# Kernel optimization log

Hardware: AMD Instinct MI355X
Metric: run time of the kernel (lower is better)

## Reference

```python
import jax, jax.numpy as jnp
import numpy as np

G = 4          # num_groups == num_kv_groups


def _proj(W, b, xf):
    # 1x1 Conv3d == per-voxel linear: xf is [b, c, N]
    return jnp.einsum('oc,bcn->bon', W, xf) + b[None, :, None]


def setup_inputs() -> dict:
    key = jax.random.key(0)
    ks = jax.random.split(key, 5)
    c = 512
    x = jax.random.normal(ks[0], (2, c, 16, 16, 16), dtype=jnp.float32)
    s = 1.0 / np.sqrt(c)
    Wq = jax.random.normal(ks[1], (c, c), dtype=jnp.float32) * s
    Wk = jax.random.normal(ks[2], (c, c), dtype=jnp.float32) * s
    Wv = jax.random.normal(ks[3], (c, c), dtype=jnp.float32) * s
    Wo = jax.random.normal(ks[4], (c, c), dtype=jnp.float32) * s
    z = jnp.zeros((c,), dtype=jnp.float32)
    return {"x": x, "Wq": Wq, "bq": z, "Wk": Wk, "bk": z, "Wv": Wv, "bv": z, "Wo": Wo, "bo": z}


def reference(x, Wq, bq, Wk, bk, Wv, bv, Wo, bo):
    b, c, d, h, w = x.shape
    N = d * h * w
    gs = c // G                       # head (group) dim
    scale = gs ** -0.5
    xf = x.reshape(b, c, N)           # [b, c, N]
    q = _proj(Wq, bq, xf).reshape(b, G, gs, N).transpose(0, 1, 3, 2)  # [b,G,N,gs]
    k = _proj(Wk, bk, xf).reshape(b, G, gs, N).transpose(0, 1, 3, 2)
    v = _proj(Wv, bv, xf).reshape(b, G, gs, N).transpose(0, 1, 3, 2)
    sim = jnp.einsum('bgqd,bgkd->bgqk', q, k) * scale  # [b,G,N,N]
    attn = jax.nn.softmax(sim, axis=-1)
    out = jnp.einsum('bgqk,bgkd->bgqd', attn, v)       # [b,G,N,gs]
    out = out.transpose(0, 1, 3, 2).reshape(b, c, N)   # [b,c,N]
    out = _proj(Wo, bo, out).reshape(b, c, d, h, w)
    return x + out
```

## Files before the change

### kernel.cpp

```cpp
#include <hip/hip_runtime.h>
#include <hip/hip_bf16.h>
#include <stdint.h>

#define B_ 2
#define C_ 512
#define G_ 4
#define D_ 128
#define N_ 4096

typedef __bf16 bf16;
typedef __bf16 bf16x8 __attribute__((ext_vector_type(8)));
typedef float  f32x4  __attribute__((ext_vector_type(4)));
typedef float  f32x16 __attribute__((ext_vector_type(16)));

#define MFMA   __builtin_amdgcn_mfma_f32_16x16x32_bf16
#define MFMA32 __builtin_amdgcn_mfma_f32_32x32x16_bf16

#define SWZ(row, c) ((((c) ^ (((row) >> 1) & 3)) << 4))

#define OFF_Q   (0u)
#define OFF_K   (8388608u)
#define OFF_VT  (16777216u)
#define OFF_XT  (25165824u)
#define OFF_WB  (33554432u)
#define OFF_OP  (35651584u)
#define OFF_ML  (52428800u)
#define WS_NEED_SPLIT (52953088u)

__device__ inline unsigned pk2(float a, float b) {
    union { bf16 h[2]; unsigned u; } t;
    t.h[0] = (bf16)a; t.h[1] = (bf16)b;
    return t.u;
}
__device__ inline void pl32(unsigned &a, unsigned &b) {
    asm volatile("v_permlane32_swap_b32 %0, %1" : "+v"(a), "+v"(b));
}
__device__ inline void gload16(const char* src, char* lds) {
    __builtin_amdgcn_global_load_lds(
        (const __attribute__((address_space(1))) unsigned*)src,
        (__attribute__((address_space(3))) unsigned*)lds, 16, 0, 0);
}
__device__ inline float max3f(float a, float b, float c) {
    return fmaxf(fmaxf(a, b), c);
}

__global__ __launch_bounds__(256) void wcvt_kernel(const float* __restrict__ Wq,
                                                   const float* __restrict__ Wk,
                                                   const float* __restrict__ Wv,
                                                   const float* __restrict__ Wo,
                                                   bf16* __restrict__ out) {
    int m = blockIdx.y;
    const float* W = (m == 0) ? Wq : (m == 1) ? Wk : (m == 2) ? Wv : Wo;
    int i = (blockIdx.x * 256 + threadIdx.x) * 4;
    float4 v = *(const float4*)(W + i);
    union { bf16 h[4]; uint2 u; } pk;
    pk.h[0] = (bf16)v.x; pk.h[1] = (bf16)v.y; pk.h[2] = (bf16)v.z; pk.h[3] = (bf16)v.w;
    *(uint2*)(out + (size_t)m * (C_ * C_) + i) = pk.u;
}

__global__ __launch_bounds__(256) void xt_kernel(const float* __restrict__ x,
                                                 bf16* __restrict__ xT) {
    __shared__ bf16 t[64 * 80];
    int n0 = blockIdx.x * 64, c0 = blockIdx.y * 64, b = blockIdx.z;
    const float* xp = x + (size_t)b * C_ * N_;
#pragma unroll
    for (int i = 0; i < 16; ++i) {
        int idx = threadIdx.x + 256 * i;
        int cl = idx >> 6, nl = idx & 63;
        float v = xp[(size_t)(c0 + cl) * N_ + n0 + nl];
        t[nl * 80 + cl] = (bf16)v;
    }
    __syncthreads();
    bf16* xt = xT + ((size_t)b * N_ + n0) * C_ + c0;
#pragma unroll
    for (int i = 0; i < 2; ++i) {
        int id = threadIdx.x + 256 * i;
        int nl = id >> 3, c8 = (id & 7) * 8;
        *(uint4*)(xt + (size_t)nl * C_ + c8) = *(const uint4*)(t + nl * 80 + c8);
    }
}

__global__ __launch_bounds__(256) void qkv_kernel(const bf16* __restrict__ xT,
                                                  const bf16* __restrict__ WB,
                                                  const float* __restrict__ bq,
                                                  const float* __restrict__ bk,
                                                  const float* __restrict__ bv,
                                                  bf16* __restrict__ Q,
                                                  bf16* __restrict__ K,
                                                  bf16* __restrict__ Vt) {
    __shared__ char smem[32768];
    const int tid = threadIdx.x;
    const int w = tid >> 6, l = tid & 63;
    const int lr = l & 15, lg = l >> 4;
    const int wr = w >> 1, wc = w & 1;
    const int mat = blockIdx.z;
    const bf16* A = xT;
    const bf16* W = WB + (size_t)mat * (C_ * C_);
    const float* bias = (mat == 0) ? bq : (mat == 1) ? bk : bv;
    const int r0 = blockIdx.x * 128, o0 = blockIdx.y * 128;
    const float QSCALE = 0.08838834764831845f * 1.4426950408889634f;

    const char* srcA[2]; const char* srcB[2]; int dA[2], dB[2];
#pragma unroll
    for (int i = 0; i < 2; ++i) {
        int CL = tid + 256 * i, row = CL >> 2, c = CL & 3;
        srcA[i] = (const char*)(A + (size_t)(r0 + row) * C_) + SWZ(row, c);
        srcB[i] = (const char*)(W + (size_t)(o0 + row) * C_) + SWZ(row, c);
        dA[i] = CL << 4;
        dB[i] = 8192 + (CL << 4);
    }

    f32x4 z = {0.f, 0.f, 0.f, 0.f};
    f32x4 acc[4][4];
#pragma unroll
    for (int m = 0; m < 4; ++m)
#pragma unroll
        for (int n = 0; n < 4; ++n) acc[m][n] = z;

    auto STAGE = [&](int buf, int kt) {
        char* base = smem + buf * 16384;
        int kb = kt * 64;
#pragma unroll
        for (int i = 0; i < 2; ++i) {
            gload16(srcA[i] + kb, base + dA[i]);
            gload16(srcB[i] + kb, base + dB[i]);
        }
    };

    STAGE(0, 0);
    __syncthreads();
#pragma unroll 4
    for (int t = 0; t < 16; ++t) {
        int cur = t & 1;
        if (t < 15) STAGE(cur ^ 1, t + 1);
        char* Ab = smem + cur * 16384;
        char* Bb = Ab + 8192;
        bf16x8 af[4], bg_[4];
#pragma unroll
        for (int m = 0; m < 4; ++m) {
            int row = wr * 64 + m * 16 + lr;
            af[m] = *(const bf16x8*)(Ab + row * 64 + SWZ(row, lg));
        }
#pragma unroll
        for (int n = 0; n < 4; ++n) {
            int row = wc * 64 + n * 16 + lr;
            bg_[n] = *(const bf16x8*)(Bb + row * 64 + SWZ(row, lg));
        }
#pragma unroll
        for (int m = 0; m < 4; ++m)
#pragma unroll
            for (int n = 0; n < 4; ++n)
                acc[m][n] = MFMA(af[m], bg_[n], acc[m][n], 0, 0, 0);
        __syncthreads();
    }

#pragma unroll
    for (int n = 0; n < 4; ++n) {
        int o = o0 + wc * 64 + n * 16 + lr;
        float bs = bias[o];
        int g = o >> 7, d = o & 127;
#pragma unroll
        for (int m = 0; m < 4; ++m) {
            int row = r0 + wr * 64 + m * 16 + lg * 4;
            int b = row >> 12, nn = row & (N_ - 1);
            if (mat == 0) {
#pragma unroll
                for (int j = 0; j < 4; ++j)
                    Q[((size_t)(b * G_ + g) * N_ + nn + j) * D_ + d] =
                        (bf16)((acc[m][n][j] + bs) * QSCALE);
            } else if (mat == 1) {
#pragma unroll
                for (int j = 0; j < 4; ++j)
                    K[((size_t)(b * G_ + g) * N_ + nn + j) * D_ + d] =
                        (bf16)(acc[m][n][j] + bs);
            } else {
                union { bf16 h[4]; uint2 u; } pk;
#pragma unroll
                for (int j = 0; j < 4; ++j) pk.h[j] = (bf16)(acc[m][n][j] + bs);
                *(uint2*)(Vt + ((size_t)(b * G_ + g) * D_ + d) * N_ + nn) = pk.u;
            }
        }
    }
}

template<int SPLITS>
__global__ __launch_bounds__(256, 2) void attn_kernel(const bf16* __restrict__ Q,
                                                      const bf16* __restrict__ K,
                                                      const bf16* __restrict__ Vt,
                                                      bf16* __restrict__ XT,
                                                      bf16* __restrict__ Op,
                                                      float* __restrict__ ML) {
    __shared__ char smem[65536];
    const int tid = threadIdx.x;
    const int w = tid >> 6, l = tid & 63;
    const int l31 = l & 31, h = l >> 5;

    const int L = blockIdx.x;
    const int bg = L & 7;
    const int ix = L >> 3;
    const int sp = (SPLITS > 1) ? (ix >> 5) : 0;
    const int qb = (SPLITS > 1) ? (ix & 31) : ix;

    const bf16* Qh = Q + (size_t)bg * N_ * D_;
    const char* Kh = (const char*)(K + (size_t)bg * N_ * D_);
    const char* Vh = (const char*)(Vt + (size_t)bg * D_ * N_);
    const int q0 = qb * 128 + w * 32;
    const int kv0 = sp * (N_ / SPLITS);
    const int NT = N_ / SPLITS / 64;

    int offK[4], offV[4];
#pragma unroll
    for (int j = 0; j < 4; ++j) {
        int CL = (w * 4 + j) * 64 + l;
        int row = CL >> 4;
        int cp = (CL & 15) ^ (row & 15);
        offK[j] = row * 256 + cp * 16;
        int dv = 2 * row + (cp >> 3), k8 = cp & 7;
        offV[j] = dv * (N_ * 2) + k8 * 16;
    }

    bf16x8 aq[8];
#pragma unroll
    for (int kb = 0; kb < 8; ++kb)
        aq[kb] = *(const bf16x8*)(Qh + (size_t)(q0 + l31) * D_ + kb * 16 + h * 8);

    bf16 one_ = (bf16)1.0f;
    bf16x8 ones = {one_, one_, one_, one_, one_, one_, one_, one_};

    f32x16 oacc[4], lacc;
#pragma unroll
    for (int dt = 0; dt < 4; ++dt)
#pragma unroll
        for (int r = 0; r < 16; ++r) oacc[dt][r] = 0.f;
#pragma unroll
    for (int r = 0; r < 16; ++r) lacc[r] = 0.f;
    float mrun = -1e30f;
    const float THR = 5.0f;

    auto STAGE = [&](int buf, int kv) {
        const char* pk = Kh + (size_t)kv * 256;
        const char* pv = Vh + (size_t)kv * 2;
        char* kb = smem + buf * 32768 + w * 4096;
        char* vb = smem + buf * 32768 + 16384 + w * 4096;
#pragma unroll
        for (int j = 0; j < 4; ++j) gload16(pk + offK[j], kb + j * 1024);
#pragma unroll
        for (int j = 0; j < 4; ++j) gload16(pv + offV[j], vb + j * 1024);
    };

    STAGE(0, kv0);

    for (int t = 0; t < NT; ++t) {
        int cur = t & 1;
        __builtin_amdgcn_s_barrier();
        if (t + 1 < NT) {
            STAGE(cur ^ 1, kv0 + (t + 1) * 64);
            asm volatile("s_waitcnt vmcnt(8)" ::: "memory");
        } else {
            asm volatile("s_waitcnt vmcnt(0)" ::: "memory");
        }
        __builtin_amdgcn_sched_barrier(0);
        __builtin_amdgcn_s_barrier();
        char* Kb = smem + cur * 32768;
        char* Vb = smem + cur * 32768 + 16384;

        f32x16 s0, s1;
#pragma unroll
        for (int r = 0; r < 16; ++r) { s0[r] = 0.f; s1[r] = 0.f; }
        __builtin_amdgcn_s_setprio(1);
#pragma unroll
        for (int kb = 0; kb < 8; ++kb) {
            int ch = (((kb << 1) | h) ^ (l31 & 15)) << 4;
            bf16x8 kf0 = *(const bf16x8*)(Kb + (size_t)l31 * 256 + ch);
            s0 = MFMA32(kf0, aq[kb], s0, 0, 0, 0);
            bf16x8 kf1 = *(const bf16x8*)(Kb + (size_t)(32 + l31) * 256 + ch);
            s1 = MFMA32(kf1, aq[kb], s1, 0, 0, 0);
        }
        __builtin_amdgcn_s_setprio(0);

        float x0 = max3f(s0[0],  s0[1],  s0[2]);
        float x1 = max3f(s0[3],  s0[4],  s0[5]);
        float x2 = max3f(s0[6],  s0[7],  s0[8]);
        float x3 = max3f(s0[9],  s0[10], s0[11]);
        float x4 = max3f(s0[12], s0[13], s0[14]);
        float x5 = max3f(s0[15], s1[0],  s1[1]);
        float x6 = max3f(s1[2],  s1[3],  s1[4]);
        float x7 = max3f(s1[5],  s1[6],  s1[7]);
        float x8 = max3f(s1[8],  s1[9],  s1[10]);
        float x9 = max3f(s1[11], s1[12], s1[13]);
        float xa = fmaxf(s1[14], s1[15]);
        float y0 = max3f(x0, x1, x2);
        float y1 = max3f(x3, x4, x5);
        float y2 = max3f(x6, x7, x8);
        float y3 = fmaxf(x9, xa);
        float mt = fmaxf(max3f(y0, y1, y2), y3);
        mt = fmaxf(mt, __shfl_xor(mt, 32));

        if (__any(mt > mrun + THR)) {
            float mn = fmaxf(mrun, mt);
            float corr = __builtin_amdgcn_exp2f(mrun - mn);
            mrun = mn;
#pragma unroll
            for (int r = 0; r < 16; ++r) {
                int qr = (r & 3) + 8 * (r >> 2) + 4 * h;
                float cr = __shfl(corr, qr);
                lacc[r] *= cr;
#pragma unroll
                for (int dt = 0; dt < 4; ++dt) oacc[dt][r] *= cr;
            }
        }

#pragma unroll
        for (int r = 0; r < 16; ++r) {
            s0[r] = __builtin_amdgcn_exp2f(s0[r] - mrun);
            s1[r] = __builtin_amdgcn_exp2f(s1[r] - mrun);
        }

        bf16x8 pa0, pa1, pa2, pa3;
        {
            unsigned x0_ = pk2(s0[0], s0[1]),  y0_ = pk2(s0[4], s0[5]);  pl32(x0_, y0_);
            unsigned x1_ = pk2(s0[2], s0[3]),  y1_ = pk2(s0[6], s0[7]);  pl32(x1_, y1_);
            pa0 = __builtin_bit_cast(bf16x8, (uint4){x0_, x1_, y0_, y1_});
            unsigned x2_ = pk2(s0[8], s0[9]),  y2_ = pk2(s0[12], s0[13]); pl32(x2_, y2_);
            unsigned x3_ = pk2(s0[10], s0[11]), y3_ = pk2(s0[14], s0[15]); pl32(x3_, y3_);
            pa1 = __builtin_bit_cast(bf16x8, (uint4){x2_, x3_, y2_, y3_});
            unsigned x4_ = pk2(s1[0], s1[1]),  y4_ = pk2(s1[4], s1[5]);  pl32(x4_, y4_);
            unsigned x5_ = pk2(s1[2], s1[3]),  y5_ = pk2(s1[6], s1[7]);  pl32(x5_, y5_);
            pa2 = __builtin_bit_cast(bf16x8, (uint4){x4_, x5_, y4_, y5_});
            unsigned x6_ = pk2(s1[8], s1[9]),  y6_ = pk2(s1[12], s1[13]); pl32(x6_, y6_);
            unsigned x7_ = pk2(s1[10], s1[11]), y7_ = pk2(s1[14], s1[15]); pl32(x7_, y7_);
            pa3 = __builtin_bit_cast(bf16x8, (uint4){x6_, x7_, y6_, y7_});
        }

        __builtin_amdgcn_s_setprio(1);
#pragma unroll
        for (int sl = 0; sl < 4; ++sl) {
            bf16x8 pa = (sl == 0) ? pa0 : (sl == 1) ? pa1 : (sl == 2) ? pa2 : pa3;
#pragma unroll
            for (int dt = 0; dt < 4; ++dt) {
                int row = dt * 16 + (l31 >> 1);
                int ch = ((((l31 & 1) << 3) + (sl << 1) + h) ^ (l31 >> 1)) << 4;
                bf16x8 vf = *(const bf16x8*)(Vb + (size_t)row * 256 + ch);
                oacc[dt] = MFMA32(pa, vf, oacc[dt], 0, 0, 0);
            }
            lacc = MFMA32(pa, ones, lacc, 0, 0, 0);
        }
        __builtin_amdgcn_s_setprio(0);
    }

    if (SPLITS > 1) {
        float2* mlp = (float2*)ML + ((size_t)sp * 8 + bg) * N_ + q0;
#pragma unroll
        for (int r = 0; r < 16; ++r) {
            int qr = (r & 3) + 8 * (r >> 2) + 4 * h;
            float mv = __shfl(mrun, qr);
            if (l31 == 0) {
                float2 v; v.x = mv; v.y = lacc[r];
                mlp[qr] = v;
            }
        }
        bf16* op = Op + (((size_t)sp * 8 + bg) * N_ + q0) * D_;
#pragma unroll
        for (int dt = 0; dt < 4; ++dt)
#pragma unroll
            for (int r = 0; r < 16; ++r) {
                int qr = (r & 3) + 8 * (r >> 2) + 4 * h;
                op[(size_t)qr * D_ + dt * 32 + l31] = (bf16)oacc[dt][r];
            }
    } else {
        int b = bg >> 2, g = bg & 3;
#pragma unroll
        for (int r = 0; r < 16; ++r) {
            int qr = (r & 3) + 8 * (r >> 2) + 4 * h;
            float iv = 1.f / lacc[r];
#pragma unroll
            for (int dt = 0; dt < 4; ++dt)
                XT[((size_t)b * N_ + q0 + qr) * C_ + g * D_ + dt * 32 + l31] =
                    (bf16)(oacc[dt][r] * iv);
        }
    }
}

__global__ __launch_bounds__(256) void merge_kernel(const bf16* __restrict__ Op,
                                                    const float* __restrict__ ML,
                                                    bf16* __restrict__ XT) {
    int t = threadIdx.x & 15, rl = threadIdx.x >> 4;
    int r = blockIdx.x * 16 + rl;
    int bg = r >> 12, n = r & (N_ - 1);
    const float2* mlp = (const float2*)ML;
    float2 ml0 = mlp[r], ml1 = mlp[32768 + r];
    float mm = fmaxf(ml0.x, ml1.x);
    float w0 = __builtin_amdgcn_exp2f(ml0.x - mm);
    float w1 = __builtin_amdgcn_exp2f(ml1.x - mm);
    float inv = 1.f / (w0 * ml0.y + w1 * ml1.y);
    w0 *= inv; w1 *= inv;
    bf16x8 o0 = *(const bf16x8*)(Op + (size_t)r * D_ + t * 8);
    bf16x8 o1 = *(const bf16x8*)(Op + (size_t)(32768 + r) * D_ + t * 8);
    union { bf16 h[8]; uint4 u; } pk;
#pragma unroll
    for (int e = 0; e < 8; ++e)
        pk.h[e] = (bf16)(w0 * (float)o0[e] + w1 * (float)o1[e]);
    int b = bg >> 2, g = bg & 3;
    *(uint4*)(XT + ((size_t)b * N_ + n) * C_ + g * D_ + t * 8) = pk.u;
}

__global__ __launch_bounds__(256) void oproj_kernel(const bf16* __restrict__ Ob,
                                                    const bf16* __restrict__ WB,
                                                    const float* __restrict__ bo,
                                                    const float* __restrict__ x,
                                                    float* __restrict__ out) {
    __shared__ char smem[24576];
    const int tid = threadIdx.x;
    const int w = tid >> 6, l = tid & 63;
    const int lr = l & 15, lg = l >> 4;
    const int wr = w >> 1, wc = w & 1;
    const bf16* W = WB + (size_t)3 * (C_ * C_);
    const int r0 = blockIdx.x * 128, o0 = blockIdx.y * 64;

    const char* srcA[2]; int dA[2];
#pragma unroll
    for (int i = 0; i < 2; ++i) {
        int CL = tid + 256 * i, row = CL >> 2, c = CL & 3;
        srcA[i] = (const char*)(Ob + (size_t)(r0 + row) * C_) + SWZ(row, c);
        dA[i] = CL << 4;
    }
    const char* srcB; int dB;
    {
        int CL = tid, row = CL >> 2, c = CL & 3;
        srcB = (const char*)(W + (size_t)(o0 + row) * C_) + SWZ(row, c);
        dB = 8192 + (CL << 4);
    }

    f32x4 z = {0.f, 0.f, 0.f, 0.f};
    f32x4 acc[4][2];
#pragma unroll
    for (int m = 0; m < 4; ++m) { acc[m][0] = z; acc[m][1] = z; }

    auto STAGE = [&](int buf, int kt) {
        char* base = smem + buf * 12288;
        int kb = kt * 64;
#pragma unroll
        for (int i = 0; i < 2; ++i) gload16(srcA[i] + kb, base + dA[i]);
        gload16(srcB + kb, base + dB);
    };

    STAGE(0, 0);
    __syncthreads();
#pragma unroll 4
    for (int t = 0; t < 16; ++t) {
        int cur = t & 1;
        if (t < 15) STAGE(cur ^ 1, t + 1);
        char* Ab = smem + cur * 12288;
        char* Bb = Ab + 8192;
        bf16x8 af[4], bg_[2];
#pragma unroll
        for (int m = 0; m < 4; ++m) {
            int row = wr * 64 + m * 16 + lr;
            af[m] = *(const bf16x8*)(Ab + row * 64 + SWZ(row, lg));
        }
#pragma unroll
        for (int n = 0; n < 2; ++n) {
            int row = wc * 32 + n * 16 + lr;
            bg_[n] = *(const bf16x8*)(Bb + row * 64 + SWZ(row, lg));
        }
#pragma unroll
        for (int m = 0; m < 4; ++m)
#pragma unroll
            for (int n = 0; n < 2; ++n)
                acc[m][n] = MFMA(af[m], bg_[n], acc[m][n], 0, 0, 0);
        __syncthreads();
    }

#pragma unroll
    for (int n = 0; n < 2; ++n) {
        int o = o0 + wc * 32 + n * 16 + lr;
        float bs = bo[o];
#pragma unroll
        for (int m = 0; m < 4; ++m) {
            int row = r0 + wr * 64 + m * 16 + lg * 4;
            int b = row >> 12, nn = row & (N_ - 1);
            size_t base = ((size_t)b * C_ + o) * N_ + nn;
            float4 xv = *(const float4*)(x + base);
            float4 ov;
            ov.x = acc[m][n][0] + bs + xv.x;
            ov.y = acc[m][n][1] + bs + xv.y;
            ov.z = acc[m][n][2] + bs + xv.z;
            ov.w = acc[m][n][3] + bs + xv.w;
            *(float4*)(out + base) = ov;
        }
    }
}

extern "C" void kernel_launch(void* const* d_in, const int* in_sizes, int n_in,
                              void* d_out, int out_size, void* d_ws, size_t ws_size,
                              hipStream_t stream) {
    const float* x  = (const float*)d_in[0];
    const float* Wq = (const float*)d_in[1];
    const float* bq = (const float*)d_in[2];
    const float* Wk = (const float*)d_in[3];
    const float* bk = (const float*)d_in[4];
    const float* Wv = (const float*)d_in[5];
    const float* bv = (const float*)d_in[6];
    const float* Wo = (const float*)d_in[7];
    const float* bo = (const float*)d_in[8];

    char* ws = (char*)d_ws;
    bf16* Q   = (bf16*)(ws + OFF_Q);
    bf16* K   = (bf16*)(ws + OFF_K);
    bf16* Vt  = (bf16*)(ws + OFF_VT);
    bf16* XT  = (bf16*)(ws + OFF_XT);
    bf16* WB  = (bf16*)(ws + OFF_WB);
    bf16* Op  = (bf16*)(ws + OFF_OP);
    float* ML = (float*)(ws + OFF_ML);
    float* out = (float*)d_out;

    hipLaunchKernelGGL(wcvt_kernel, dim3(256, 4), dim3(256), 0, stream, Wq, Wk, Wv, Wo, WB);
    hipLaunchKernelGGL(xt_kernel, dim3(64, 8, 2), dim3(256), 0, stream, x, XT);
    hipLaunchKernelGGL(qkv_kernel, dim3(64, 4, 3), dim3(256), 0, stream,
                       XT, WB, bq, bk, bv, Q, K, Vt);
    if (ws_size >= (size_t)WS_NEED_SPLIT) {
        hipLaunchKernelGGL(attn_kernel<2>, dim3(512), dim3(256), 0, stream,
                           Q, K, Vt, XT, Op, ML);
        hipLaunchKernelGGL(merge_kernel, dim3(2048), dim3(256), 0, stream, Op, ML, XT);
    } else {
        hipLaunchKernelGGL(attn_kernel<1>, dim3(256), dim3(256), 0, stream,
                           Q, K, Vt, XT, Op, ML);
    }
    hipLaunchKernelGGL(oproj_kernel, dim3(64, 8), dim3(256), 0, stream, XT, WB, bo, x, out);
}
```

Baseline: 137.2 us.

## Software-pipeline QK^T one tile ahead of softmax and PV in attention loop

Splits K and V staging into separate double buffers and computes the next tile's QK^T scores before the current tile's softmax and PV MFMAs. The aim is to let the independent MFMA work for S(t+1) overlap the exp/max VALU work of tile t, and to prefetch K two tiles ahead. This costs an extra 32 accumulator registers (sN0/sN1), which may lower occupancy or cause spills, and makes the wait-count logic more complex.

```diff
diff --git a/kernel.cpp b/kernel.cpp
--- a/kernel.cpp
+++ b/kernel.cpp
@@ -237,58 +237,83 @@
     float mrun = -1e30f;
     const float THR = 5.0f;
 
-    auto STAGE = [&](int buf, int kv) {
+    auto STAGE_K = [&](int buf, int kv) {
         const char* pk = Kh + (size_t)kv * 256;
+        char* kb = smem + buf * 16384 + w * 4096;
+#pragma unroll
+        for (int j = 0; j < 4; ++j) gload16(pk + offK[j], kb + j * 1024);
+    };
+    auto STAGE_V = [&](int buf, int kv) {
         const char* pv = Vh + (size_t)kv * 2;
-        char* kb = smem + buf * 32768 + w * 4096;
-        char* vb = smem + buf * 32768 + 16384 + w * 4096;
-#pragma unroll
-        for (int j = 0; j < 4; ++j) gload16(pk + offK[j], kb + j * 1024);
+        char* vb = smem + 32768 + buf * 16384 + w * 4096;
 #pragma unroll
         for (int j = 0; j < 4; ++j) gload16(pv + offV[j], vb + j * 1024);
     };
 
-    STAGE(0, kv0);
-
-    for (int t = 0; t < NT; ++t) {
-        int cur = t & 1;
-        __builtin_amdgcn_s_barrier();
-        if (t + 1 < NT) {
-            STAGE(cur ^ 1, kv0 + (t + 1) * 64);
-            asm volatile("s_waitcnt vmcnt(8)" ::: "memory");
-        } else {
-            asm volatile("s_waitcnt vmcnt(0)" ::: "memory");
-        }
-        __builtin_amdgcn_sched_barrier(0);
-        __builtin_amdgcn_s_barrier();
-        char* Kb = smem + cur * 32768;
-        char* Vb = smem + cur * 32768 + 16384;
-
-        f32x16 s0, s1;
-#pragma unroll
-        for (int r = 0; r < 16; ++r) { s0[r] = 0.f; s1[r] = 0.f; }
+    STAGE_K(0, kv0);
+    STAGE_V(0, kv0);
+    if (NT > 1) STAGE_K(1, kv0 + 64);
+    if (NT > 1) asm volatile("s_waitcnt vmcnt(8)" ::: "memory");
+    else        asm volatile("s_waitcnt vmcnt(4)" ::: "memory");
+    __builtin_amdgcn_sched_barrier(0);
+    __builtin_amdgcn_s_barrier();
+
+    f32x16 sP0, sP1, sN0, sN1;
+    {
+        char* Kb = smem;
+#pragma unroll
+        for (int r = 0; r < 16; ++r) { sP0[r] = 0.f; sP1[r] = 0.f; }
         __builtin_amdgcn_s_setprio(1);
 #pragma unroll
         for (int kb = 0; kb < 8; ++kb) {
             int ch = (((kb << 1) | h) ^ (l31 & 15)) << 4;
             bf16x8 kf0 = *(const bf16x8*)(Kb + (size_t)l31 * 256 + ch);
-            s0 = MFMA32(kf0, aq[kb], s0, 0, 0, 0);
+            sP0 = MFMA32(kf0, aq[kb], sP0, 0, 0, 0);
             bf16x8 kf1 = *(const bf16x8*)(Kb + (size_t)(32 + l31) * 256 + ch);
-            s1 = MFMA32(kf1, aq[kb], s1, 0, 0, 0);
+            sP1 = MFMA32(kf1, aq[kb], sP1, 0, 0, 0);
         }
         __builtin_amdgcn_s_setprio(0);
-
-        float x0 = max3f(s0[0],  s0[1],  s0[2]);
-        float x1 = max3f(s0[3],  s0[4],  s0[5]);
-        float x2 = max3f(s0[6],  s0[7],  s0[8]);
-        float x3 = max3f(s0[9],  s0[10], s0[11]);
-        float x4 = max3f(s0[12], s0[13], s0[14]);
-        float x5 = max3f(s0[15], s1[0],  s1[1]);
-        float x6 = max3f(s1[2],  s1[3],  s1[4]);
-        float x7 = max3f(s1[5],  s1[6],  s1[7]);
-        float x8 = max3f(s1[8],  s1[9],  s1[10]);
-        float x9 = max3f(s1[11], s1[12], s1[13]);
-        float xa = fmaxf(s1[14], s1[15]);
+    }
+
+#pragma unroll 2
+    for (int t = 0; t < NT; ++t) {
+        const int p = t & 1, q = p ^ 1;
+        __builtin_amdgcn_s_barrier();
+        if (t + 2 < NT) STAGE_K(p, kv0 + (t + 2) * 64);
+        if (t + 1 < NT) STAGE_V(q, kv0 + (t + 1) * 64);
+        if (t + 2 < NT)      asm volatile("s_waitcnt vmcnt(8)" ::: "memory");
+        else if (t + 1 < NT) asm volatile("s_waitcnt vmcnt(4)" ::: "memory");
+        else                 asm volatile("s_waitcnt vmcnt(0)" ::: "memory");
+        __builtin_amdgcn_sched_barrier(0);
+        __builtin_amdgcn_s_barrier();
+
+        if (t + 1 < NT) {
+            char* Kb = smem + q * 16384;
+#pragma unroll
+            for (int r = 0; r < 16; ++r) { sN0[r] = 0.f; sN1[r] = 0.f; }
+            __builtin_amdgcn_s_setprio(1);
+#pragma unroll
+            for (int kb = 0; kb < 8; ++kb) {
+                int ch = (((kb << 1) | h) ^ (l31 & 15)) << 4;
+                bf16x8 kf0 = *(const bf16x8*)(Kb + (size_t)l31 * 256 + ch);
+                sN0 = MFMA32(kf0, aq[kb], sN0, 0, 0, 0);
+                bf16x8 kf1 = *(const bf16x8*)(Kb + (size_t)(32 + l31) * 256 + ch);
+                sN1 = MFMA32(kf1, aq[kb], sN1, 0, 0, 0);
+            }
+            __builtin_amdgcn_s_setprio(0);
+        }
+
+        float x0 = max3f(sP0[0],  sP0[1],  sP0[2]);
+        float x1 = max3f(sP0[3],  sP0[4],  sP0[5]);
+        float x2 = max3f(sP0[6],  sP0[7],  sP0[8]);
+        float x3 = max3f(sP0[9],  sP0[10], sP0[11]);
+        float x4 = max3f(sP0[12], sP0[13], sP0[14]);
+        float x5 = max3f(sP0[15], sP1[0],  sP1[1]);
+        float x6 = max3f(sP1[2],  sP1[3],  sP1[4]);
+        float x7 = max3f(sP1[5],  sP1[6],  sP1[7]);
+        float x8 = max3f(sP1[8],  sP1[9],  sP1[10]);
+        float x9 = max3f(sP1[11], sP1[12], sP1[13]);
+        float xa = fmaxf(sP1[14], sP1[15]);
         float y0 = max3f(x0, x1, x2);
         float y1 = max3f(x3, x4, x5);
         float y2 = max3f(x6, x7, x8);
@@ -312,26 +337,27 @@
 
 #pragma unroll
         for (int r = 0; r < 16; ++r) {
-            s0[r] = __builtin_amdgcn_exp2f(s0[r] - mrun);
-            s1[r] = __builtin_amdgcn_exp2f(s1[r] - mrun);
+            sP0[r] = __builtin_amdgcn_exp2f(sP0[r] - mrun);
+            sP1[r] = __builtin_amdgcn_exp2f(sP1[r] - mrun);
         }
 
         bf16x8 pa0, pa1, pa2, pa3;
         {
-            unsigned x0_ = pk2(s0[0], s0[1]),  y0_ = pk2(s0[4], s0[5]);  pl32(x0_, y0_);
-            unsigned x1_ = pk2(s0[2], s0[3]),  y1_ = pk2(s0[6], s0[7]);  pl32(x1_, y1_);
+            unsigned x0_ = pk2(sP0[0], sP0[1]),  y0_ = pk2(sP0[4], sP0[5]);  pl32(x0_, y0_);
+            unsigned x1_ = pk2(sP0[2], sP0[3]),  y1_ = pk2(sP0[6], sP0[7]);  pl32(x1_, y1_);
             pa0 = __builtin_bit_cast(bf16x8, (uint4){x0_, x1_, y0_, y1_});
-            unsigned x2_ = pk2(s0[8], s0[9]),  y2_ = pk2(s0[12], s0[13]); pl32(x2_, y2_);
-            unsigned x3_ = pk2(s0[10], s0[11]), y3_ = pk2(s0[14], s0[15]); pl32(x3_, y3_);
+            unsigned x2_ = pk2(sP0[8], sP0[9]),  y2_ = pk2(sP0[12], sP0[13]); pl32(x2_, y2_);
+            unsigned x3_ = pk2(sP0[10], sP0[11]), y3_ = pk2(sP0[14], sP0[15]); pl32(x3_, y3_);
             pa1 = __builtin_bit_cast(bf16x8, (uint4){x2_, x3_, y2_, y3_});
-            unsigned x4_ = pk2(s1[0], s1[1]),  y4_ = pk2(s1[4], s1[5]);  pl32(x4_, y4_);
-            unsigned x5_ = pk2(s1[2], s1[3]),  y5_ = pk2(s1[6], s1[7]);  pl32(x5_, y5_);
+            unsigned x4_ = pk2(sP1[0], sP1[1]),  y4_ = pk2(sP1[4], sP1[5]);  pl32(x4_, y4_);
+            unsigned x5_ = pk2(sP1[2], sP1[3]),  y5_ = pk2(sP1[6], sP1[7]);  pl32(x5_, y5_);
             pa2 = __builtin_bit_cast(bf16x8, (uint4){x4_, x5_, y4_, y5_});
-            unsigned x6_ = pk2(s1[8], s1[9]),  y6_ = pk2(s1[12], s1[13]); pl32(x6_, y6_);
-            unsigned x7_ = pk2(s1[10], s1[11]), y7_ = pk2(s1[14], s1[15]); pl32(x7_, y7_);
+            unsigned x6_ = pk2(sP1[8], sP1[9]),  y6_ = pk2(sP1[12], sP1[13]); pl32(x6_, y6_);
+            unsigned x7_ = pk2(sP1[10], sP1[11]), y7_ = pk2(sP1[14], sP1[15]); pl32(x7_, y7_);
             pa3 = __builtin_bit_cast(bf16x8, (uint4){x6_, x7_, y6_, y7_});
         }
 
+        char* Vb = smem + 32768 + p * 16384;
         __builtin_amdgcn_s_setprio(1);
 #pragma unroll
         for (int sl = 0; sl < 4; ++sl) {
@@ -346,6 +372,8 @@
             lacc = MFMA32(pa, ones, lacc, 0, 0, 0);
         }
         __builtin_amdgcn_s_setprio(0);
+
+        sP0 = sN0; sP1 = sN1;
     }
 
     if (SPLITS > 1) {
```

New measurement: 137.7 us. Within noise of the previous version (+0.4%).
